# Performance work log

Hardware: AMD Instinct MI355X
Metric: run time of the kernel (lower is better)

The kernel has to match this reference:

```python
import jax, jax.numpy as jnp
import numpy as np

N_NODES = 50000
N_EDGES = 500000
F_DIM = 128
N_REL = 8
N_LAYERS = 2
NEG_SLOPE = 0.2  # PyG RGATConv default negative_slope


def setup_inputs() -> dict:
    key = jax.random.key(0)
    ks = jax.random.split(key, 6)
    x = jax.random.normal(ks[0], (N_NODES, F_DIM), dtype=jnp.float32)
    edge_index = jax.random.randint(ks[1], (2, N_EDGES), 0, N_NODES)
    edge_type = jax.random.randint(ks[2], (N_EDGES,), 0, N_REL)
    # Per-layer relation weights [L, R, F_in, F_out], attention vectors q,k [L, F_out, 1], bias [L, F_out]
    W = jax.random.normal(ks[3], (N_LAYERS, N_REL, F_DIM, F_DIM), dtype=jnp.float32) * (1.0 / np.sqrt(F_DIM)).astype(np.float32)
    att_q = jax.random.normal(ks[4], (N_LAYERS, F_DIM, 1), dtype=jnp.float32) * 0.1
    att_k = jax.random.normal(ks[5], (N_LAYERS, F_DIM, 1), dtype=jnp.float32) * 0.1
    bias = jnp.zeros((N_LAYERS, F_DIM), dtype=jnp.float32)
    return {"x": x, "W": W, "att_q": att_q, "att_k": att_k, "bias": bias,
            "edge_index": edge_index, "edge_type": edge_type}


def _segment_softmax(logits, seg, num_segments):
    # Numerically stable softmax over edges grouped by destination node.
    m = jax.ops.segment_max(logits, seg, num_segments=num_segments)
    m = jax.lax.stop_gradient(m)
    e = jnp.exp(logits - m[seg])
    denom = jax.ops.segment_sum(e, seg, num_segments=num_segments)
    return e / (denom[seg] + 1e-16)


def _rgat_layer(h, src, dst, edge_type, W, q, k, b):
    # h: [N, F]; W: [R, F, F]. Project once per relation, then gather per edge
    # (avoids materializing [E, F, F] per-edge weight gathers).
    n = h.shape[0]
    xw = jnp.einsum('nf,rfg->rng', h, W)          # [R, N, F]
    out_j = xw[edge_type, src]                    # [E, F] transformed source feats
    out_i = xw[edge_type, dst]                    # [E, F] transformed dest feats
    # additive self-attention: leaky_relu(q(x_i) + k(x_j)), heads=1, dim=1
    logits = jax.nn.leaky_relu((out_i @ q + out_j @ k)[:, 0], NEG_SLOPE)  # [E]
    alpha = _segment_softmax(logits, dst, n)      # across-relation softmax per dst node
    agg = jax.ops.segment_sum(alpha[:, None] * out_j, dst, num_segments=n)  # [N, F]
    return agg + b


def reference(x, W, att_q, att_k, bias, edge_index, edge_type):
    src, dst = edge_index[0], edge_index[1]
    h = x
    for l in range(W.shape[0]):  # small fixed layer count
        h = _rgat_layer(h, src, dst, edge_type, W[l], att_q[l], att_k[l], bias[l])
        h = jax.nn.relu(h)  # dropout is identity in eval mode
    return h
```

## Files before the change

kernel.cpp:

```cpp
#include <hip/hip_runtime.h>
#include <hip/hip_bf16.h>
#include <hip/hip_fp16.h>

#define N_NODES 50000
#define N_EDGES 500000
#define F_DIM   128
#define N_REL   8
#define N_LAYERS 2
#define NEG_SLOPE 0.2f

#define NBLK_N ((N_NODES + 255) / 256)

typedef _Float16 half8 __attribute__((ext_vector_type(8)));
typedef float f32x4  __attribute__((ext_vector_type(4)));


__device__ inline float lrelu(float l) { return (l > 0.f) ? l : NEG_SLOPE * l; }

__global__ __launch_bounds__(256) void prep_h(const float* __restrict__ H,
                                              _Float16* __restrict__ Hf) {
    const size_t i8 = (size_t)blockIdx.x * 256 + threadIdx.x;
    if (i8 >= (size_t)N_NODES * F_DIM / 8) return;
    const float* src = H + i8 * 8;
    float av[8];
    *(float4*)(av)     = *(const float4*)(src);
    *(float4*)(av + 4) = *(const float4*)(src + 4);
    alignas(16) _Float16 hb[8];
#pragma unroll
    for (int j = 0; j < 8; ++j) hb[j] = (_Float16)av[j];
    *(uint4*)(Hf + i8 * 8) = *(const uint4*)hb;
}

__global__ __launch_bounds__(256) void prep_w(const float* __restrict__ W,
                                              _Float16* __restrict__ Wf) {
    __shared__ float tile[64][F_DIM + 1];
    const int mat = blockIdx.x;
    const float* src = W + (size_t)mat * F_DIM * F_DIM;
    const int t = threadIdx.x;
    for (int hf = 0; hf < 2; ++hf) {
#pragma unroll
        for (int i = 0; i < 8; ++i) {
            int idx = t + i * 256;
            int f = idx >> 5, c4 = idx & 31;
            float4 v = *(const float4*)(src + (size_t)(hf * 64 + f) * F_DIM + c4 * 4);
            *(float4*)&tile[f][c4 * 4] = v;
        }
        __syncthreads();
        int g = t >> 1, fs = (t & 1) * 32;
        for (int c = 0; c < 4; ++c) {
            alignas(16) _Float16 th[8];
#pragma unroll
            for (int j = 0; j < 8; ++j) th[j] = (_Float16)tile[fs + c * 8 + j][g];
            size_t o = ((size_t)mat * F_DIM + g) * F_DIM + hf * 64 + fs + c * 8;
            *(uint4*)(Wf + o) = *(const uint4*)th;
        }
        __syncthreads();
    }
}

#define GBM 128
#define RGRP 2
__global__ __launch_bounds__(256, 2) void gemm_xw(const _Float16* __restrict__ Hf,
                                                  const _Float16* __restrict__ Wf,
                                                  const float* __restrict__ qv_g,
                                                  const float* __restrict__ kv_g,
                                                  const unsigned char* __restrict__ used,
                                                  __half* __restrict__ xw,
                                                  float* __restrict__ a_q,
                                                  float* __restrict__ a_k) {
    __shared__ _Float16 lds[F_DIM * F_DIM];
    const int rb0 = blockIdx.x * GBM;
    const int r0  = blockIdx.y * RGRP;
    const int tid = threadIdx.x;
    const int lane = tid & 63, w = tid >> 6;
    const int q = lane >> 4, ln = lane & 15;

    half8 Af[2][4];
#pragma unroll
    for (int rt = 0; rt < 2; ++rt) {
        int row = rb0 + w * 32 + rt * 16 + ln;
        int ar = (row < N_NODES) ? row : (N_NODES - 1);
        const _Float16* hp = Hf + (size_t)ar * F_DIM;
#pragma unroll
        for (int ks = 0; ks < 4; ++ks)
            Af[rt][ks] = *(const half8*)(hp + ks * 32 + q * 8);
    }

    float qvl[8], kvl[8];
#pragma unroll
    for (int t = 0; t < 8; ++t) {
        qvl[t] = qv_g[t * 16 + ln];
        kvl[t] = kv_g[t * 16 + ln];
    }

    for (int rr = 0; rr < RGRP; ++rr) {
        const int r = r0 + rr;
        __syncthreads();
        {
            const _Float16* src = Wf + (size_t)r * F_DIM * F_DIM;
#pragma unroll
            for (int i = 0; i < 8; ++i) {
                int chunk = tid + i * 256;
                int gg = chunk >> 4, c8 = chunk & 15;
                uint4 v = *(const uint4*)(src + gg * F_DIM + c8 * 8);
                *(uint4*)(lds + gg * F_DIM + ((c8 ^ (gg & 15)) * 8)) = v;
            }
        }
        __syncthreads();

        f32x4 acc[2][8];
#pragma unroll
        for (int rt = 0; rt < 2; ++rt)
#pragma unroll
            for (int t = 0; t < 8; ++t) acc[rt][t] = (f32x4)(0.f);

#pragma unroll
        for (int ks = 0; ks < 4; ++ks) {
            const int jx = (((ks * 4 + q) ^ ln)) << 3;
            half8 Bf[8];
#pragma unroll
            for (int c = 0; c < 8; ++c)
                Bf[c] = *(const half8*)(lds + (c * 16 + ln) * F_DIM + jx);
#pragma unroll
            for (int c = 0; c < 8; ++c)
#pragma unroll
                for (int rt = 0; rt < 2; ++rt)
                    acc[rt][c] = __builtin_amdgcn_mfma_f32_16x16x32_f16(Af[rt][ks], Bf[c], acc[rt][c], 0, 0, 0);
        }

#pragma unroll
        for (int rt = 0; rt < 2; ++rt) {
            float pq[4], pk[4];
#pragma unroll
            for (int reg = 0; reg < 4; ++reg) {
                const int row = rb0 + w * 32 + rt * 16 + q * 4 + reg;
                alignas(16) unsigned short hs[8];
                float sq = 0.f, sk = 0.f;
#pragma unroll
                for (int t = 0; t < 8; ++t) {
                    float v = acc[rt][t][reg];
                    __half hv = __float2half(v);
                    hs[t] = *reinterpret_cast<unsigned short*>(&hv);
                    sq = fmaf(v, qvl[t], sq);
                    sk = fmaf(v, kvl[t], sk);
                }
                if (row < N_NODES && used[(size_t)r * N_NODES + row])
                    *(uint4*)(xw + ((size_t)r * N_NODES + row) * F_DIM + ln * 8) = *(const uint4*)hs;
                pq[reg] = sq; pk[reg] = sk;
            }
#pragma unroll
            for (int reg = 0; reg < 4; ++reg) {
#pragma unroll
                for (int m = 1; m <= 8; m <<= 1) {
                    pq[reg] += __shfl_xor(pq[reg], m);
                    pk[reg] += __shfl_xor(pk[reg], m);
                }
            }
            if (ln == 0) {
#pragma unroll
                for (int reg = 0; reg < 4; ++reg) {
                    const int row = rb0 + w * 32 + rt * 16 + q * 4 + reg;
                    if (row < N_NODES) {
                        a_q[r * N_NODES + row] = pq[reg];
                        a_k[r * N_NODES + row] = pk[reg];
                    }
                }
            }
        }
    }
}


__global__ __launch_bounds__(256) void count_kernel(const int* __restrict__ dstp,
                                                    int* __restrict__ cnt) {
    int e = blockIdx.x * 256 + threadIdx.x;
    if (e < N_EDGES) atomicAdd(cnt + dstp[e], 1);
}

__global__ __launch_bounds__(256) void block_sum_kernel(const int* __restrict__ cnt,
                                                        int* __restrict__ partial) {
    __shared__ int s[256];
    int idx = blockIdx.x * 256 + threadIdx.x;
    int v = (idx < N_NODES) ? cnt[idx] : 0;
    s[threadIdx.x] = v;
    __syncthreads();
    for (int off = 128; off > 0; off >>= 1) {
        if (threadIdx.x < off) s[threadIdx.x] += s[threadIdx.x + off];
        __syncthreads();
    }
    if (threadIdx.x == 0) partial[blockIdx.x] = s[0];
}

__global__ __launch_bounds__(256) void scan_partials_kernel(int* __restrict__ partial,
                                                            int* __restrict__ row_ptr) {
    __shared__ int s[256];
    int t = threadIdx.x;
    int v = (t < NBLK_N) ? partial[t] : 0;
    s[t] = v;
    __syncthreads();
#pragma unroll
    for (int off = 1; off < 256; off <<= 1) {
        int x = (t >= off) ? s[t - off] : 0;
        __syncthreads();
        s[t] += x;
        __syncthreads();
    }
    if (t < NBLK_N) partial[t] = s[t] - v;
    if (t == 0) row_ptr[N_NODES] = N_EDGES;
}

__global__ __launch_bounds__(256) void scan_block_kernel(const int* __restrict__ cnt,
                                                         const int* __restrict__ partial,
                                                         int* __restrict__ row_ptr) {
    __shared__ int s[256];
    int t = threadIdx.x;
    int idx = blockIdx.x * 256 + t;
    int v = (idx < N_NODES) ? cnt[idx] : 0;
    s[t] = v;
    __syncthreads();
#pragma unroll
    for (int off = 1; off < 256; off <<= 1) {
        int x = (t >= off) ? s[t - off] : 0;
        __syncthreads();
        s[t] += x;
        __syncthreads();
    }
    if (idx < N_NODES) row_ptr[idx] = partial[blockIdx.x] + s[t] - v;
}

__global__ __launch_bounds__(256) void scatter_kernel(const int* __restrict__ srcp,
                                                      const int* __restrict__ dstp,
                                                      const int* __restrict__ etp,
                                                      const int* __restrict__ row_ptr,
                                                      int* __restrict__ cnt,
                                                      unsigned* __restrict__ sorted,
                                                      unsigned char* __restrict__ used) {
    int e = blockIdx.x * 256 + threadIdx.x;
    if (e >= N_EDGES) return;
    int d = dstp[e], s = srcp[e], t = etp[e];
    int pos = atomicSub(cnt + d, 1) - 1;
    sorted[row_ptr[d] + pos] = (unsigned)s | ((unsigned)t << 16);
    used[(size_t)t * N_NODES + s] = 1;
}

__device__ inline void accum8(float* acc, uint4 v, float a) {
    const __half2* h2 = reinterpret_cast<const __half2*>(&v);
#pragma unroll
    for (int t = 0; t < 4; ++t) {
        float2 f = __half22float2(h2[t]);
        acc[t * 2]     = fmaf(a, f.x, acc[t * 2]);
        acc[t * 2 + 1] = fmaf(a, f.y, acc[t * 2 + 1]);
    }
}
__device__ inline const uint4* xwrow(const __half* xw, unsigned p, int ln) {
    return (const uint4*)(xw + (((size_t)(p >> 16)) * N_NODES + (p & 0xffff)) * F_DIM + ln * 8);
}

__global__ __launch_bounds__(256) void agg_fused(const __half* __restrict__ xw,
                                                 const float* __restrict__ a_q,
                                                 const float* __restrict__ a_k,
                                                 const int* __restrict__ row_ptr,
                                                 const unsigned* __restrict__ sorted,
                                                 const float* __restrict__ bias,
                                                 float* __restrict__ out) {
    const int lane = threadIdx.x & 63;
    const int wave = threadIdx.x >> 6;
    const int d = blockIdx.x * 4 + wave;
    if (d >= N_NODES) return;
    const int beg = row_ptr[d], end = row_ptr[d + 1];
    const int cnt = end - beg;
    const int g = lane >> 4, ln = lane & 15;

    if (cnt <= 64) {
        unsigned p = 0;
        float l = -3.4e38f;
        if (lane < cnt) {
            p = sorted[beg + lane];
            int s = p & 0xffff, t = p >> 16;
            l = lrelu(a_q[t * N_NODES + d] + a_k[t * N_NODES + s]);
        }
        float m = l;
#pragma unroll
        for (int off = 32; off > 0; off >>= 1) m = fmaxf(m, __shfl_xor(m, off));
        float ex = (lane < cnt) ? __expf(l - m) : 0.f;
        float dsum = ex;
#pragma unroll
        for (int off = 32; off > 0; off >>= 1) dsum += __shfl_xor(dsum, off);
        const float alpha = ex / (dsum + 1e-16f);

        float acc[8] = {0, 0, 0, 0, 0, 0, 0, 0};
        for (int i = 0; i < cnt; i += 8) {
            unsigned p0 = __shfl(p, i + g);
            unsigned p1 = __shfl(p, i + 4 + g);
            float a0 = __shfl(alpha, i + g);
            float a1 = __shfl(alpha, i + 4 + g);
            uint4 v0 = *xwrow(xw, p0, ln);
            uint4 v1 = *xwrow(xw, p1, ln);
            accum8(acc, v0, a0);
            accum8(acc, v1, a1);
        }
#pragma unroll
        for (int t = 0; t < 8; ++t) {
            acc[t] += __shfl_xor(acc[t], 16);
            acc[t] += __shfl_xor(acc[t], 32);
        }
        if (g == 0) {
#pragma unroll
            for (int t = 0; t < 8; ++t) {
                const int col = t * 16 + ln;
                out[(size_t)d * F_DIM + col] = fmaxf(acc[t] + bias[col], 0.f);
            }
        }
    } else {
        const int p0 = lane * 2;
        const int c0 = (p0 & 7) * 16 + (p0 >> 3);
        const int c1 = c0 + 16;
        float2 acc = make_float2(bias[c0], bias[c1]);
        float m = -3.4e38f;
        for (int i = beg + lane; i < end; i += 64) {
            unsigned p = sorted[i];
            int s = p & 0xffff, t = p >> 16;
            m = fmaxf(m, lrelu(a_q[t * N_NODES + d] + a_k[t * N_NODES + s]));
        }
#pragma unroll
        for (int off = 32; off > 0; off >>= 1) m = fmaxf(m, __shfl_xor(m, off));
        float dsum = 0.f;
        for (int i = beg + lane; i < end; i += 64) {
            unsigned p = sorted[i];
            int s = p & 0xffff, t = p >> 16;
            dsum += __expf(lrelu(a_q[t * N_NODES + d] + a_k[t * N_NODES + s]) - m);
        }
#pragma unroll
        for (int off = 32; off > 0; off >>= 1) dsum += __shfl_xor(dsum, off);
        const float inv = 1.f / (dsum + 1e-16f);
        for (int i = beg; i < end; ++i) {
            unsigned p = sorted[i];
            int s = p & 0xffff, t = p >> 16;
            float alpha = __expf(lrelu(a_q[t * N_NODES + d] + a_k[t * N_NODES + s]) - m) * inv;
            const __half2 h2 = *((const __half2*)xw + (((size_t)(p >> 16)) * N_NODES + (p & 0xffff)) * (F_DIM / 2) + lane);
            float2 v = make_float2(__half2float(h2.x), __half2float(h2.y));
            acc.x = fmaf(alpha, v.x, acc.x);
            acc.y = fmaf(alpha, v.y, acc.y);
        }
        out[(size_t)d * F_DIM + c0] = fmaxf(acc.x, 0.f);
        out[(size_t)d * F_DIM + c1] = fmaxf(acc.y, 0.f);
    }
}


extern "C" void kernel_launch(void* const* d_in, const int* in_sizes, int n_in,
                              void* d_out, int out_size, void* d_ws, size_t ws_size,
                              hipStream_t stream) {
    const float* x     = (const float*)d_in[0];
    const float* W     = (const float*)d_in[1];
    const float* att_q = (const float*)d_in[2];
    const float* att_k = (const float*)d_in[3];
    const float* bias  = (const float*)d_in[4];
    const int* ei      = (const int*)d_in[5];
    const int* etp     = (const int*)d_in[6];
    const int* srcp = ei;
    const int* dstp = ei + N_EDGES;
    float* out = (float*)d_out;
    char* ws   = (char*)d_ws;

    size_t off = 0;
    auto alloc = [&](size_t bytes) {
        void* p = ws + off;
        off = (off + bytes + 511) & ~(size_t)511;
        return p;
    };
    __half* xw       = (__half*)alloc((size_t)N_REL * N_NODES * F_DIM * sizeof(__half));
    float* a_q       = (float*)alloc((size_t)N_REL * N_NODES * sizeof(float));
    float* a_k       = (float*)alloc((size_t)N_REL * N_NODES * sizeof(float));
    const size_t cnt_bytes  = (size_t)N_NODES * sizeof(int);
    const size_t cnt_pad    = (cnt_bytes + 511) & ~(size_t)511;
    const size_t used_bytes = (size_t)N_REL * N_NODES;
    char* zeroblk    = (char*)alloc(cnt_pad + used_bytes);
    int* cnt         = (int*)zeroblk;
    unsigned char* used = (unsigned char*)(zeroblk + cnt_pad);
    int* row_ptr     = (int*)alloc(((size_t)N_NODES + 1) * sizeof(int));
    int* partial     = (int*)alloc(256 * sizeof(int));
    unsigned* sorted = (unsigned*)alloc((size_t)N_EDGES * sizeof(unsigned));
    _Float16* Wf     = (_Float16*)alloc((size_t)N_LAYERS * N_REL * F_DIM * F_DIM * sizeof(_Float16));
    _Float16* Hf     = (_Float16*)alloc((size_t)N_NODES * F_DIM * sizeof(_Float16));

    prep_w<<<N_LAYERS * N_REL, 256, 0, stream>>>(W, Wf);
    hipMemsetAsync(zeroblk, 0, cnt_pad + used_bytes, stream);
    count_kernel<<<(N_EDGES + 255) / 256, 256, 0, stream>>>(dstp, cnt);
    block_sum_kernel<<<NBLK_N, 256, 0, stream>>>(cnt, partial);
    scan_partials_kernel<<<1, 256, 0, stream>>>(partial, row_ptr);
    scan_block_kernel<<<NBLK_N, 256, 0, stream>>>(cnt, partial, row_ptr);
    scatter_kernel<<<(N_EDGES + 255) / 256, 256, 0, stream>>>(
        srcp, dstp, etp, row_ptr, cnt, sorted, used);

    const int grid_h = (N_NODES * F_DIM / 8 + 255) / 256;
    const int grid_m = (N_NODES + GBM - 1) / GBM;
    for (int l = 0; l < N_LAYERS; ++l) {
        const float* H = (l == 0) ? x : out;
        prep_h<<<grid_h, 256, 0, stream>>>(H, Hf);
        gemm_xw<<<dim3(grid_m, N_REL / RGRP), 256, 0, stream>>>(
            Hf, Wf + (size_t)l * N_REL * F_DIM * F_DIM,
            att_q + l * F_DIM, att_k + l * F_DIM, used,
            xw, a_q, a_k);
        agg_fused<<<(N_NODES + 3) / 4, 256, 0, stream>>>(
            xw, a_q, a_k, row_ptr, sorted, bias + l * F_DIM, out);
    }
}
```

Before: 300.3 us.

## Fold attention vectors into weights, fuse prep kernels and single-block scan

Precomputes W·q and W·k per relation so the attention logits come from an extra MFMA column in the GEMM instead of per-row FMAs and shuffles. It merges the weight and input fp16 conversion into one kernel and replaces the three-kernel prefix scan with a single 1024-thread block. The aggregation kernel now writes the fp16 copy of the layer output directly, removing the second prep_h launch. Rounding q·W and k·W to fp16 slightly changes logit precision, and the single-block scan serialises work on one CU.

New measurement: 395.4 us. 31.7% more time.

```diff
diff --git a/kernel.cpp b/kernel.cpp
--- a/kernel.cpp
+++ b/kernel.cpp
@@ -9,52 +9,80 @@
 #define N_LAYERS 2
 #define NEG_SLOPE 0.2f
 
-#define NBLK_N ((N_NODES + 255) / 256)
-
 typedef _Float16 half8 __attribute__((ext_vector_type(8)));
 typedef float f32x4  __attribute__((ext_vector_type(4)));
 
 
 __device__ inline float lrelu(float l) { return (l > 0.f) ? l : NEG_SLOPE * l; }
 
-__global__ __launch_bounds__(256) void prep_h(const float* __restrict__ H,
-                                              _Float16* __restrict__ Hf) {
-    const size_t i8 = (size_t)blockIdx.x * 256 + threadIdx.x;
-    if (i8 >= (size_t)N_NODES * F_DIM / 8) return;
-    const float* src = H + i8 * 8;
-    float av[8];
-    *(float4*)(av)     = *(const float4*)(src);
-    *(float4*)(av + 4) = *(const float4*)(src + 4);
-    alignas(16) _Float16 hb[8];
-#pragma unroll
-    for (int j = 0; j < 8; ++j) hb[j] = (_Float16)av[j];
-    *(uint4*)(Hf + i8 * 8) = *(const uint4*)hb;
-}
-
-__global__ __launch_bounds__(256) void prep_w(const float* __restrict__ W,
-                                              _Float16* __restrict__ Wf) {
-    __shared__ float tile[64][F_DIM + 1];
-    const int mat = blockIdx.x;
-    const float* src = W + (size_t)mat * F_DIM * F_DIM;
+#define NPREP_H ((N_NODES * F_DIM / 8 + 255) / 256)
+__global__ __launch_bounds__(256) void prep_all(const float* __restrict__ W,
+                                                const float* __restrict__ x,
+                                                const float* __restrict__ att_q,
+                                                const float* __restrict__ att_k,
+                                                _Float16* __restrict__ Wf,
+                                                _Float16* __restrict__ wq,
+                                                _Float16* __restrict__ wk,
+                                                _Float16* __restrict__ Hf) {
     const int t = threadIdx.x;
-    for (int hf = 0; hf < 2; ++hf) {
-#pragma unroll
-        for (int i = 0; i < 8; ++i) {
-            int idx = t + i * 256;
-            int f = idx >> 5, c4 = idx & 31;
-            float4 v = *(const float4*)(src + (size_t)(hf * 64 + f) * F_DIM + c4 * 4);
-            *(float4*)&tile[f][c4 * 4] = v;
-        }
-        __syncthreads();
-        int g = t >> 1, fs = (t & 1) * 32;
-        for (int c = 0; c < 4; ++c) {
-            alignas(16) _Float16 th[8];
-#pragma unroll
-            for (int j = 0; j < 8; ++j) th[j] = (_Float16)tile[fs + c * 8 + j][g];
-            size_t o = ((size_t)mat * F_DIM + g) * F_DIM + hf * 64 + fs + c * 8;
-            *(uint4*)(Wf + o) = *(const uint4*)th;
-        }
-        __syncthreads();
+    if (blockIdx.x < N_LAYERS * N_REL) {
+        __shared__ float tile[64][F_DIM + 1];
+        const int mat = blockIdx.x;
+        const int l = mat >> 3;
+        const float* src = W + (size_t)mat * F_DIM * F_DIM;
+        const float* qv = att_q + l * F_DIM;
+        const float* kv = att_k + l * F_DIM;
+        for (int hf = 0; hf < 2; ++hf) {
+#pragma unroll
+            for (int i = 0; i < 8; ++i) {
+                int idx = t + i * 256;
+                int f = idx >> 5, c4 = idx & 31;
+                float4 v = *(const float4*)(src + (size_t)(hf * 64 + f) * F_DIM + c4 * 4);
+                *(float4*)&tile[f][c4 * 4] = v;
+            }
+            __syncthreads();
+            {
+                int g = t >> 1, fs = (t & 1) * 32;
+                for (int c = 0; c < 4; ++c) {
+                    alignas(16) _Float16 th[8];
+#pragma unroll
+                    for (int j = 0; j < 8; ++j) th[j] = (_Float16)tile[fs + c * 8 + j][g];
+                    size_t o = ((size_t)mat * F_DIM + g) * F_DIM + hf * 64 + fs + c * 8;
+                    *(uint4*)(Wf + o) = *(const uint4*)th;
+                }
+            }
+            {
+                int fl = t >> 2, seg = t & 3;
+                float pq = 0.f, pk = 0.f;
+#pragma unroll
+                for (int g4 = 0; g4 < 8; ++g4) {
+                    int g = seg * 32 + g4 * 4;
+                    float4 wv = *(const float4*)(&tile[fl][g]);
+                    float4 q4 = *(const float4*)(qv + g);
+                    float4 k4 = *(const float4*)(kv + g);
+                    pq += wv.x * q4.x + wv.y * q4.y + wv.z * q4.z + wv.w * q4.w;
+                    pk += wv.x * k4.x + wv.y * k4.y + wv.z * k4.z + wv.w * k4.w;
+                }
+                pq += __shfl_xor(pq, 1); pq += __shfl_xor(pq, 2);
+                pk += __shfl_xor(pk, 1); pk += __shfl_xor(pk, 2);
+                if (seg == 0) {
+                    wq[(size_t)mat * F_DIM + hf * 64 + fl] = (_Float16)pq;
+                    wk[(size_t)mat * F_DIM + hf * 64 + fl] = (_Float16)pk;
+                }
+            }
+            __syncthreads();
+        }
+    } else {
+        const size_t i8 = (size_t)(blockIdx.x - N_LAYERS * N_REL) * 256 + t;
+        if (i8 >= (size_t)N_NODES * F_DIM / 8) return;
+        const float* src = x + i8 * 8;
+        float av[8];
+        *(float4*)(av)     = *(const float4*)(src);
+        *(float4*)(av + 4) = *(const float4*)(src + 4);
+        alignas(16) _Float16 hb[8];
+#pragma unroll
+        for (int j = 0; j < 8; ++j) hb[j] = (_Float16)av[j];
+        *(uint4*)(Hf + i8 * 8) = *(const uint4*)hb;
     }
 }
 
@@ -62,8 +90,8 @@
 #define RGRP 2
 __global__ __launch_bounds__(256, 2) void gemm_xw(const _Float16* __restrict__ Hf,
                                                   const _Float16* __restrict__ Wf,
-                                                  const float* __restrict__ qv_g,
-                                                  const float* __restrict__ kv_g,
+                                                  const _Float16* __restrict__ wq,
+                                                  const _Float16* __restrict__ wk,
                                                   const unsigned char* __restrict__ used,
                                                   __half* __restrict__ xw,
                                                   float* __restrict__ a_q,
@@ -86,12 +114,7 @@
             Af[rt][ks] = *(const half8*)(hp + ks * 32 + q * 8);
     }
 
-    float qvl[8], kvl[8];
-#pragma unroll
-    for (int t = 0; t < 8; ++t) {
-        qvl[t] = qv_g[t * 16 + ln];
-        kvl[t] = kv_g[t * 16 + ln];
-    }
+    const half8 hzero = (half8)(_Float16)0.f;
 
     for (int rr = 0; rr < RGRP; ++rr) {
         const int r = r0 + rr;
@@ -108,11 +131,17 @@
         }
         __syncthreads();
 
+        const _Float16* wqr = wq + (size_t)r * F_DIM;
+        const _Float16* wkr = wk + (size_t)r * F_DIM;
+
         f32x4 acc[2][8];
-#pragma unroll
-        for (int rt = 0; rt < 2; ++rt)
+        f32x4 acc_qk[2];
+#pragma unroll
+        for (int rt = 0; rt < 2; ++rt) {
 #pragma unroll
             for (int t = 0; t < 8; ++t) acc[rt][t] = (f32x4)(0.f);
+            acc_qk[rt] = (f32x4)(0.f);
+        }
 
 #pragma unroll
         for (int ks = 0; ks < 4; ++ks) {
@@ -121,49 +150,39 @@
 #pragma unroll
             for (int c = 0; c < 8; ++c)
                 Bf[c] = *(const half8*)(lds + (c * 16 + ln) * F_DIM + jx);
+            half8 Bqk = hzero;
+            if (ln == 0)      Bqk = *(const half8*)(wqr + ks * 32 + q * 8);
+            else if (ln == 1) Bqk = *(const half8*)(wkr + ks * 32 + q * 8);
 #pragma unroll
             for (int c = 0; c < 8; ++c)
 #pragma unroll
                 for (int rt = 0; rt < 2; ++rt)
                     acc[rt][c] = __builtin_amdgcn_mfma_f32_16x16x32_f16(Af[rt][ks], Bf[c], acc[rt][c], 0, 0, 0);
+#pragma unroll
+            for (int rt = 0; rt < 2; ++rt)
+                acc_qk[rt] = __builtin_amdgcn_mfma_f32_16x16x32_f16(Af[rt][ks], Bqk, acc_qk[rt], 0, 0, 0);
         }
 
 #pragma unroll
         for (int rt = 0; rt < 2; ++rt) {
-            float pq[4], pk[4];
 #pragma unroll
             for (int reg = 0; reg < 4; ++reg) {
                 const int row = rb0 + w * 32 + rt * 16 + q * 4 + reg;
                 alignas(16) unsigned short hs[8];
-                float sq = 0.f, sk = 0.f;
 #pragma unroll
                 for (int t = 0; t < 8; ++t) {
-                    float v = acc[rt][t][reg];
-                    __half hv = __float2half(v);
+                    __half hv = __float2half(acc[rt][t][reg]);
                     hs[t] = *reinterpret_cast<unsigned short*>(&hv);
-                    sq = fmaf(v, qvl[t], sq);
-                    sk = fmaf(v, kvl[t], sk);
                 }
                 if (row < N_NODES && used[(size_t)r * N_NODES + row])
                     *(uint4*)(xw + ((size_t)r * N_NODES + row) * F_DIM + ln * 8) = *(const uint4*)hs;
-                pq[reg] = sq; pk[reg] = sk;
-            }
-#pragma unroll
-            for (int reg = 0; reg < 4; ++reg) {
-#pragma unroll
-                for (int m = 1; m <= 8; m <<= 1) {
-                    pq[reg] += __shfl_xor(pq[reg], m);
-                    pk[reg] += __shfl_xor(pk[reg], m);
-                }
-            }
-            if (ln == 0) {
+            }
+            if (ln < 2) {
+                float* dst = (ln == 0) ? a_q : a_k;
 #pragma unroll
                 for (int reg = 0; reg < 4; ++reg) {
                     const int row = rb0 + w * 32 + rt * 16 + q * 4 + reg;
-                    if (row < N_NODES) {
-                        a_q[r * N_NODES + row] = pq[reg];
-                        a_k[r * N_NODES + row] = pk[reg];
-                    }
+                    if (row < N_NODES) dst[r * N_NODES + row] = acc_qk[rt][reg];
                 }
             }
         }
@@ -177,55 +196,34 @@
     if (e < N_EDGES) atomicAdd(cnt + dstp[e], 1);
 }
 
-__global__ __launch_bounds__(256) void block_sum_kernel(const int* __restrict__ cnt,
-                                                        int* __restrict__ partial) {
-    __shared__ int s[256];
-    int idx = blockIdx.x * 256 + threadIdx.x;
-    int v = (idx < N_NODES) ? cnt[idx] : 0;
-    s[threadIdx.x] = v;
+__global__ __launch_bounds__(1024) void scan_all(const int* __restrict__ cnt,
+                                                 int* __restrict__ row_ptr) {
+    __shared__ int part[1024];
+    const int t = threadIdx.x;
+    const int CH = (N_NODES + 1023) >> 10;
+    const int base = t * CH;
+    int s = 0;
+    for (int i = 0; i < CH; ++i) {
+        int idx = base + i;
+        if (idx < N_NODES) s += cnt[idx];
+    }
+    part[t] = s;
     __syncthreads();
-    for (int off = 128; off > 0; off >>= 1) {
-        if (threadIdx.x < off) s[threadIdx.x] += s[threadIdx.x + off];
+    for (int off = 1; off < 1024; off <<= 1) {
+        int v = (t >= off) ? part[t - off] : 0;
         __syncthreads();
-    }
-    if (threadIdx.x == 0) partial[blockIdx.x] = s[0];
-}
-
-__global__ __launch_bounds__(256) void scan_partials_kernel(int* __restrict__ partial,
-                                                            int* __restrict__ row_ptr) {
-    __shared__ int s[256];
-    int t = threadIdx.x;
-    int v = (t < NBLK_N) ? partial[t] : 0;
-    s[t] = v;
-    __syncthreads();
-#pragma unroll
-    for (int off = 1; off < 256; off <<= 1) {
-        int x = (t >= off) ? s[t - off] : 0;
+        part[t] += v;
         __syncthreads();
-        s[t] += x;
-        __syncthreads();
-    }
-    if (t < NBLK_N) partial[t] = s[t] - v;
+    }
+    int pre = part[t] - s;
+    for (int i = 0; i < CH; ++i) {
+        int idx = base + i;
+        if (idx < N_NODES) {
+            row_ptr[idx] = pre;
+            pre += cnt[idx];
+        }
+    }
     if (t == 0) row_ptr[N_NODES] = N_EDGES;
-}
-
-__global__ __launch_bounds__(256) void scan_block_kernel(const int* __restrict__ cnt,
-                                                         const int* __restrict__ partial,
-                                                         int* __restrict__ row_ptr) {
-    __shared__ int s[256];
-    int t = threadIdx.x;
-    int idx = blockIdx.x * 256 + t;
-    int v = (idx < N_NODES) ? cnt[idx] : 0;
-    s[t] = v;
-    __syncthreads();
-#pragma unroll
-    for (int off = 1; off < 256; off <<= 1) {
-        int x = (t >= off) ? s[t - off] : 0;
-        __syncthreads();
-        s[t] += x;
-        __syncthreads();
-    }
-    if (idx < N_NODES) row_ptr[idx] = partial[blockIdx.x] + s[t] - v;
 }
 
 __global__ __launch_bounds__(256) void scatter_kernel(const int* __restrict__ srcp,
@@ -262,7 +260,9 @@
                                                  const int* __restrict__ row_ptr,
                                                  const unsigned* __restrict__ sorted,
                                                  const float* __restrict__ bias,
-                                                 float* __restrict__ out) {
+                                                 float* __restrict__ out,
+                                                 _Float16* __restrict__ Hf_out,
+                                                 int write_hf) {
     const int lane = threadIdx.x & 63;
     const int wave = threadIdx.x >> 6;
     const int d = blockIdx.x * 4 + wave;
@@ -308,7 +308,9 @@
 #pragma unroll
             for (int t = 0; t < 8; ++t) {
                 const int col = t * 16 + ln;
-                out[(size_t)d * F_DIM + col] = fmaxf(acc[t] + bias[col], 0.f);
+                float v = fmaxf(acc[t] + bias[col], 0.f);
+                out[(size_t)d * F_DIM + col] = v;
+                if (write_hf) Hf_out[(size_t)d * F_DIM + col] = (_Float16)v;
             }
         }
     } else {
@@ -342,8 +344,13 @@
             acc.x = fmaf(alpha, v.x, acc.x);
             acc.y = fmaf(alpha, v.y, acc.y);
         }
-        out[(size_t)d * F_DIM + c0] = fmaxf(acc.x, 0.f);
-        out[(size_t)d * F_DIM + c1] = fmaxf(acc.y, 0.f);
+        float v0 = fmaxf(acc.x, 0.f), v1 = fmaxf(acc.y, 0.f);
+        out[(size_t)d * F_DIM + c0] = v0;
+        out[(size_t)d * F_DIM + c1] = v1;
+        if (write_hf) {
+            Hf_out[(size_t)d * F_DIM + c0] = (_Float16)v0;
+            Hf_out[(size_t)d * F_DIM + c1] = (_Float16)v1;
+        }
     }
 }
 
@@ -379,30 +386,28 @@
     int* cnt         = (int*)zeroblk;
     unsigned char* used = (unsigned char*)(zeroblk + cnt_pad);
     int* row_ptr     = (int*)alloc(((size_t)N_NODES + 1) * sizeof(int));
-    int* partial     = (int*)alloc(256 * sizeof(int));
     unsigned* sorted = (unsigned*)alloc((size_t)N_EDGES * sizeof(unsigned));
     _Float16* Wf     = (_Float16*)alloc((size_t)N_LAYERS * N_REL * F_DIM * F_DIM * sizeof(_Float16));
+    _Float16* wq     = (_Float16*)alloc((size_t)N_LAYERS * N_REL * F_DIM * sizeof(_Float16));
+    _Float16* wk     = (_Float16*)alloc((size_t)N_LAYERS * N_REL * F_DIM * sizeof(_Float16));
     _Float16* Hf     = (_Float16*)alloc((size_t)N_NODES * F_DIM * sizeof(_Float16));
 
-    prep_w<<<N_LAYERS * N_REL, 256, 0, stream>>>(W, Wf);
+    prep_all<<<N_LAYERS * N_REL + NPREP_H, 256, 0, stream>>>(
+        W, x, att_q, att_k, Wf, wq, wk, Hf);
     hipMemsetAsync(zeroblk, 0, cnt_pad + used_bytes, stream);
     count_kernel<<<(N_EDGES + 255) / 256, 256, 0, stream>>>(dstp, cnt);
-    block_sum_kernel<<<NBLK_N, 256, 0, stream>>>(cnt, partial);
-    scan_partials_kernel<<<1, 256, 0, stream>>>(partial, row_ptr);
-    scan_block_kernel<<<NBLK_N, 256, 0, stream>>>(cnt, partial, row_ptr);
+    scan_all<<<1, 1024, 0, stream>>>(cnt, row_ptr);
     scatter_kernel<<<(N_EDGES + 255) / 256, 256, 0, stream>>>(
         srcp, dstp, etp, row_ptr, cnt, sorted, used);
 
-    const int grid_h = (N_NODES * F_DIM / 8 + 255) / 256;
     const int grid_m = (N_NODES + GBM - 1) / GBM;
     for (int l = 0; l < N_LAYERS; ++l) {
-        const float* H = (l == 0) ? x : out;
-        prep_h<<<grid_h, 256, 0, stream>>>(H, Hf);
         gemm_xw<<<dim3(grid_m, N_REL / RGRP), 256, 0, stream>>>(
             Hf, Wf + (size_t)l * N_REL * F_DIM * F_DIM,
-            att_q + l * F_DIM, att_k + l * F_DIM, used,
-            xw, a_q, a_k);
+            wq + (size_t)l * N_REL * F_DIM, wk + (size_t)l * N_REL * F_DIM,
+            used, xw, a_q, a_k);
         agg_fused<<<(N_NODES + 3) / 4, 256, 0, stream>>>(
-            xw, a_q, a_k, row_ptr, sorted, bias + l * F_DIM, out);
-    }
-}
+            xw, a_q, a_k, row_ptr, sorted, bias + l * F_DIM, out,
+            Hf, (l == 0) ? 1 : 0);
+    }
+}
```
